# Performance work log

Measured on AMD Instinct MI355X. Metric: run time of the kernel, lower is better.

The kernel has to match this reference:

```python
import jax, jax.numpy as jnp
import numpy as np
from jax.scipy.special import logsumexp

VOCAB, NLABEL, NSTATE = 32000, 16, 64
BATCH, MAXLEN = 512, 512


def setup_inputs() -> dict:
    key = jax.random.key(0)
    k1, k2, k3, k4, k5 = jax.random.split(key, 5)
    sentences = jax.random.randint(k1, (BATCH, MAXLEN), 0, VOCAB)
    length = jax.random.randint(k2, (BATCH,), 1, MAXLEN + 1)  # valid lengths in [1, MAXLEN]
    # parameters, uniform(-0.5, 0.5) as in reset_parameter()
    emb = jax.random.uniform(k3, (VOCAB, NSTATE), minval=-0.5, maxval=0.5, dtype=jnp.float32)
    transition = jax.random.uniform(k4, (NSTATE, NSTATE), minval=-0.5, maxval=0.5, dtype=jnp.float32)
    output = jax.random.uniform(k5, (NLABEL, NSTATE), minval=-0.5, maxval=0.5, dtype=jnp.float32)
    return {"sentences": sentences, "length": length, "emb": emb,
            "transition": transition, "output": output}


def reference(sentences, length, emb, transition, output):
    batch = sentences.shape[0]
    # emission log-probs per timestep: [T, B, S]
    emission = jax.nn.log_softmax(emb[sentences.T], axis=-1)
    trans = jax.nn.log_softmax(transition, axis=-1)  # [S, S]

    def step(f, e):
        # log-space matrix-vector product: logsumexp over previous state
        nf = logsumexp(trans[None, :, :] + f[:, None, :], axis=-1) + e  # [B, S]
        return nf, nf

    f0 = emission[0]
    _, rest = jax.lax.scan(step, f0, emission[1:])
    forwards = jnp.concatenate([f0[None], rest], axis=0)  # [T, B, S]
    hidden = forwards[length - 1, jnp.arange(batch)]  # [B, S]
    out_log = jax.nn.log_softmax(output, axis=-1)  # [L, S]
    score = logsumexp(out_log[None, :, :] + hidden[:, None, :], axis=-1)  # [B, L]
    return score
```

## Files before the change

kernel.cpp:

```cpp
#include <hip/hip_runtime.h>
#include <stdint.h>

#define VOCAB  32000
#define NSTATE 64
#define NLABEL 16
#define BATCH  512
#define MAXLEN 512

#define LOG2E 1.44269504088896340736f
#define LN2_D 0.69314718055994530942

typedef float v2f __attribute__((ext_vector_type(2)));

#if defined(__has_builtin) && __has_builtin(__builtin_amdgcn_exp2f)
#define EXP2(x) __builtin_amdgcn_exp2f(x)
#else
#define EXP2(x) exp2f(x)
#endif
#if defined(__has_builtin) && __has_builtin(__builtin_amdgcn_logf)
#define LOG2(x) __builtin_amdgcn_logf(x)
#else
#define LOG2(x) log2f(x)
#endif

#define SBAR() __builtin_amdgcn_sched_barrier(0)

__device__ __forceinline__ float wave_max64(float x) {
#pragma unroll
  for (int off = 32; off > 0; off >>= 1) x = fmaxf(x, __shfl_xor(x, off, 64));
  return x;
}
__device__ __forceinline__ float wave_sum64(float x) {
#pragma unroll
  for (int off = 32; off > 0; off >>= 1) x += __shfl_xor(x, off, 64);
  return x;
}
__device__ __forceinline__ float bcast0(float x) {
  return __uint_as_float(__builtin_amdgcn_readfirstlane(__float_as_uint(x)));
}

__global__ void prep_emb_k(const float* __restrict__ emb, float* __restrict__ emb2) {
  const int w = blockIdx.x * 4 + (threadIdx.x >> 6);
  const int s = threadIdx.x & 63;
  const float v = emb[w * NSTATE + s] * LOG2E;
  const float m = wave_max64(v);
  const float ss = wave_sum64(EXP2(v - m));
  emb2[w * NSTATE + s] = v - m - LOG2(ss);
}

__global__ void prep_mats_k(const float* __restrict__ trans, const float* __restrict__ outp,
                            float* __restrict__ W, float* __restrict__ out2) {
  const int r = blockIdx.x, s = threadIdx.x;
  if (r < NSTATE) {
    const float v = trans[r * NSTATE + s] * LOG2E;
    const float m = wave_max64(v);
    const float ss = wave_sum64(EXP2(v - m));
    W[r * NSTATE + s] = EXP2(v - m - LOG2(ss));
  } else {
    const int l = r - NSTATE;
    const float v = outp[l * NSTATE + s] * LOG2E;
    const float m = wave_max64(v);
    const float ss = wave_sum64(EXP2(v - m));
    out2[l * NSTATE + s] = v - m - LOG2(ss);
  }
}

template <bool PRE>
__global__ __launch_bounds__(64) void iohmm_fwd(
    const int* __restrict__ sents, const int* __restrict__ length,
    const float* __restrict__ emb, const float* __restrict__ trans,
    const float* __restrict__ outp, const float* __restrict__ emb2,
    const float* __restrict__ W, const float* __restrict__ out2,
    float* __restrict__ score) {
  const int b = blockIdx.x;
  const int s = threadIdx.x;
  __shared__ __align__(16) float p_lds[2][NSTATE];
  __shared__ __align__(16) int s_ids[MAXLEN];

  {
    const int4* s4 = reinterpret_cast<const int4*>(sents + b * MAXLEN);
    int4 c0 = s4[s];
    int4 c1 = s4[64 + s];
    reinterpret_cast<int4*>(s_ids)[s] = c0;
    reinterpret_cast<int4*>(s_ids)[64 + s] = c1;
  }

  v2f w2[NSTATE / 2];
  if (PRE) {
#pragma unroll
    for (int j = 0; j < 16; ++j) {
      const float4 q = *reinterpret_cast<const float4*>(W + s * NSTATE + 4 * j);
      w2[2 * j + 0] = v2f{q.x, q.y};
      w2[2 * j + 1] = v2f{q.z, q.w};
    }
  } else {
    float wr[NSTATE];
#pragma unroll
    for (int j = 0; j < 16; ++j) {
      const float4 q = *reinterpret_cast<const float4*>(trans + s * NSTATE + 4 * j);
      wr[4 * j + 0] = q.x * LOG2E; wr[4 * j + 1] = q.y * LOG2E;
      wr[4 * j + 2] = q.z * LOG2E; wr[4 * j + 3] = q.w * LOG2E;
    }
    float m = -1e30f;
#pragma unroll
    for (int j = 0; j < NSTATE; ++j) m = fmaxf(m, wr[j]);
    float ss = 0.f;
#pragma unroll
    for (int j = 0; j < NSTATE; ++j) ss += EXP2(wr[j] - m);
    const float d = m + LOG2(ss);
#pragma unroll
    for (int j = 0; j < NSTATE / 2; ++j)
      w2[j] = v2f{EXP2(wr[2 * j] - d), EXP2(wr[2 * j + 1] - d)};
  }

  const int len = length[b];
  __syncthreads();

  auto EMIT = [&](int t) -> float {
    const int tc = t < MAXLEN ? t : MAXLEN - 1;
    const int id = s_ids[tc];
    return PRE ? emb2[id * NSTATE + s] : emb[id * NSTATE + s] * LOG2E;
  };

  float e0 = EMIT(0);
  if (!PRE) {
    const float dm = wave_max64(e0);
    const float dsum = wave_sum64(EXP2(e0 - dm));
    e0 = e0 - dm - LOG2(dsum);
  }
  const float se0 = bcast0(e0);
  float p = EXP2(e0 - se0);
  double MU = (double)se0;
  int MUi = 0;

  float eA = EMIT(1);
  float eB = EMIT(2);
  float eC = EMIT(3);

  for (int t = 1; t < len; ++t) {
    float* pb = p_lds[t & 1];
    pb[s] = p;
    SBAR();

    const float eN = EMIT(t + 3);

    const float4* pb4 = reinterpret_cast<const float4*>(pb);
    v2f A0{0.f, 0.f}, A1 = A0, A2 = A0, A3 = A0, A4 = A0, A5 = A0, A6 = A0, A7 = A0;
#pragma unroll
    for (int j = 0; j < 4; ++j) {
      const float4 qa = pb4[4 * j + 0];
      const float4 qb = pb4[4 * j + 1];
      const float4 qc = pb4[4 * j + 2];
      const float4 qd = pb4[4 * j + 3];
      A0 = __builtin_elementwise_fma(w2[8 * j + 0], v2f{qa.x, qa.y}, A0);
      A1 = __builtin_elementwise_fma(w2[8 * j + 1], v2f{qa.z, qa.w}, A1);
      A2 = __builtin_elementwise_fma(w2[8 * j + 2], v2f{qb.x, qb.y}, A2);
      A3 = __builtin_elementwise_fma(w2[8 * j + 3], v2f{qb.z, qb.w}, A3);
      A4 = __builtin_elementwise_fma(w2[8 * j + 4], v2f{qc.x, qc.y}, A4);
      A5 = __builtin_elementwise_fma(w2[8 * j + 5], v2f{qc.z, qc.w}, A5);
      A6 = __builtin_elementwise_fma(w2[8 * j + 6], v2f{qd.x, qd.y}, A6);
      A7 = __builtin_elementwise_fma(w2[8 * j + 7], v2f{qd.z, qd.w}, A7);
    }
    const v2f S0 = A0 + A4, S1 = A1 + A5, S2 = A2 + A6, S3 = A3 + A7;
    const v2f T0 = S0 + S2, T1 = S1 + S3;
    const v2f U = T0 + T1;
    const float sum = U.x + U.y;
    SBAR();

    float e;
    if (PRE) {
      e = eA;
    } else {
      const float dm = wave_max64(eA);
      const float dsum = wave_sum64(EXP2(eA - dm));
      e = eA - dm - LOG2(dsum);
    }
    const float se = bcast0(e);
    const float q = EXP2(e - se);
    p = sum * q;

    if ((t & 15) == 0) {
      const uint32_t u = __builtin_amdgcn_readfirstlane(__float_as_uint(p));
      const int ex = (int)((u >> 23) & 255u) - 127;
      const float r = __uint_as_float((uint32_t)(127 - ex) << 23);
      p *= r;
      MUi += ex;
    }

    MU += (double)se;
    eA = eB; eB = eC; eC = eN;
  }

  const float f = LOG2(p);
  const double MUt = MU + (double)MUi;
  for (int l = 0; l < NLABEL; ++l) {
    float y;
    if (PRE) {
      y = out2[l * NSTATE + s] + f;
    } else {
      const float v = outp[l * NSTATE + s] * LOG2E;
      const float lm = wave_max64(v);
      const float lsum = wave_sum64(EXP2(v - lm));
      y = v - lm - LOG2(lsum) + f;
    }
    const float m = wave_max64(y);
    const float ssum = wave_sum64(EXP2(y - m));
    if (s == 0) {
      const double sc = MUt + (double)m + (double)LOG2(ssum);
      score[b * NLABEL + l] = (float)(sc * LN2_D);
    }
  }
}

extern "C" void kernel_launch(void* const* d_in, const int* in_sizes, int n_in,
                              void* d_out, int out_size, void* d_ws, size_t ws_size,
                              hipStream_t stream) {
  const int* sents = (const int*)d_in[0];
  const int* length = (const int*)d_in[1];
  const float* emb = (const float*)d_in[2];
  const float* trans = (const float*)d_in[3];
  const float* outp = (const float*)d_in[4];
  float* score = (float*)d_out;

  const size_t emb2_bytes = (size_t)VOCAB * NSTATE * sizeof(float);
  const size_t W_off = emb2_bytes;
  const size_t out2_off = W_off + NSTATE * NSTATE * sizeof(float);
  const size_t need = out2_off + NLABEL * NSTATE * sizeof(float);

  if (ws_size >= need) {
    float* emb2 = (float*)d_ws;
    float* W = (float*)((char*)d_ws + W_off);
    float* out2 = (float*)((char*)d_ws + out2_off);
    prep_emb_k<<<VOCAB / 4, 256, 0, stream>>>(emb, emb2);
    prep_mats_k<<<NSTATE + NLABEL, 64, 0, stream>>>(trans, outp, W, out2);
    iohmm_fwd<true><<<BATCH, 64, 0, stream>>>(sents, length, emb, trans, outp,
                                              emb2, W, out2, score);
  } else {
    iohmm_fwd<false><<<BATCH, 64, 0, stream>>>(sents, length, emb, trans, outp,
                                               nullptr, nullptr, nullptr, score);
  }
}
```

Measured before the change: 269.8 us.

## Precompute per-step emission factors and process two sequences per wave

Adds a prepass that gathers the emission log-probs for every (batch, timestep), converts them to linear-scale factors laid out transposed in chunks of 16 steps, and separately sums the per-step max offsets in double. The main recurrence then streams these contiguous float4 chunks with double-buffered prefetch and runs two batch elements per 64-thread block, interleaving two independent dot products to hide LDS and dependency latency. This removes the per-step dependent gather of emb2 from the serial loop. In exchange it needs a large extra workspace (about 64 MB of qT) plus two extra kernel launches, and the grid drops to 256 blocks, which run to the longer of each pair's lengths.

```diff
diff --git a/kernel.cpp b/kernel.cpp
--- a/kernel.cpp
+++ b/kernel.cpp
@@ -6,6 +6,7 @@
 #define NLABEL 16
 #define BATCH  512
 #define MAXLEN 512
+#define NCHUNK (MAXLEN / 16)
 
 #define LOG2E 1.44269504088896340736f
 #define LN2_D 0.69314718055994530942
@@ -37,6 +38,13 @@
 }
 __device__ __forceinline__ float bcast0(float x) {
   return __uint_as_float(__builtin_amdgcn_readfirstlane(__float_as_uint(x)));
+}
+__device__ __forceinline__ double shfl_xor_d(double x, int off) {
+  union { double d; int i[2]; } u;
+  u.d = x;
+  u.i[0] = __shfl_xor(u.i[0], off, 64);
+  u.i[1] = __shfl_xor(u.i[1], off, 64);
+  return u.d;
 }
 
 __global__ void prep_emb_k(const float* __restrict__ emb, float* __restrict__ emb2) {
@@ -65,8 +73,218 @@
   }
 }
 
+__global__ void prep_gather_k(const int* __restrict__ sents,
+                              const float* __restrict__ emb2,
+                              float* __restrict__ qT, float* __restrict__ mu) {
+  const int b = blockIdx.x >> 3;
+  const int tile = blockIdx.x & 7;
+  const int s = threadIdx.x;
+  __shared__ float tileb[64][65];
+
+  const int* sentrow = sents + b * MAXLEN + tile * 64;
+#pragma unroll 4
+  for (int tt = 0; tt < 64; ++tt) {
+    const int id = sentrow[tt];
+    const float e = emb2[id * NSTATE + s];
+    const float e0 = bcast0(e);
+    tileb[tt][s] = EXP2(e - e0);
+    if (s == 0) mu[b * MAXLEN + tile * 64 + tt] = e;
+  }
+  __syncthreads();
+
+  const int lt = s;
+  const int chunk = tile * 4 + (lt >> 4);
+  const int tc = lt & 15;
+  float* dst = qT + ((size_t)(b * NCHUNK + chunk) * NSTATE) * 16 + tc;
+#pragma unroll 8
+  for (int i = 0; i < NSTATE; ++i) {
+    dst[(size_t)i * 16] = tileb[lt][i];
+  }
+}
+
+__global__ void prep_musum_k(const float* __restrict__ mu, const int* __restrict__ length,
+                             double* __restrict__ musum) {
+  const int b = blockIdx.x;
+  const int lane = threadIdx.x;
+  const int len = length[b];
+  double acc = 0.0;
+#pragma unroll
+  for (int k = 0; k < 8; ++k) {
+    const int t = k * 64 + lane;
+    const float v = mu[b * MAXLEN + t];
+    if (t < len) acc += (double)v;
+  }
+#pragma unroll
+  for (int off = 32; off > 0; off >>= 1) acc += shfl_xor_d(acc, off);
+  if (lane == 0) musum[b] = acc;
+}
+
+__device__ __forceinline__ float dot64(const float* __restrict__ pl,
+                                       const v2f* __restrict__ w2) {
+  const float4* pb4 = reinterpret_cast<const float4*>(pl);
+  v2f A0{0.f, 0.f}, A1 = A0, A2 = A0, A3 = A0, A4 = A0, A5 = A0, A6 = A0, A7 = A0;
+#pragma unroll
+  for (int j = 0; j < 4; ++j) {
+    const float4 qa = pb4[4 * j + 0];
+    const float4 qb = pb4[4 * j + 1];
+    const float4 qc = pb4[4 * j + 2];
+    const float4 qd = pb4[4 * j + 3];
+    A0 = __builtin_elementwise_fma(w2[8 * j + 0], v2f{qa.x, qa.y}, A0);
+    A1 = __builtin_elementwise_fma(w2[8 * j + 1], v2f{qa.z, qa.w}, A1);
+    A2 = __builtin_elementwise_fma(w2[8 * j + 2], v2f{qb.x, qb.y}, A2);
+    A3 = __builtin_elementwise_fma(w2[8 * j + 3], v2f{qb.z, qb.w}, A3);
+    A4 = __builtin_elementwise_fma(w2[8 * j + 4], v2f{qc.x, qc.y}, A4);
+    A5 = __builtin_elementwise_fma(w2[8 * j + 5], v2f{qc.z, qc.w}, A5);
+    A6 = __builtin_elementwise_fma(w2[8 * j + 6], v2f{qd.x, qd.y}, A6);
+    A7 = __builtin_elementwise_fma(w2[8 * j + 7], v2f{qd.z, qd.w}, A7);
+  }
+  const v2f S0 = A0 + A4, S1 = A1 + A5, S2 = A2 + A6, S3 = A3 + A7;
+  const v2f T0 = S0 + S2, T1 = S1 + S3;
+  const v2f U = T0 + T1;
+  return U.x + U.y;
+}
+
+__global__ __launch_bounds__(64, 1) void iohmm_fwd3(
+    const int* __restrict__ length, const float* __restrict__ W,
+    const float* __restrict__ out2, const float* __restrict__ qT,
+    const double* __restrict__ musum, float* __restrict__ score) {
+  const int b0 = blockIdx.x * 2;
+  const int b1 = b0 + 1;
+  const int s = threadIdx.x;
+  __shared__ __align__(16) float pl0[NSTATE];
+  __shared__ __align__(16) float pl1[NSTATE];
+
+  v2f w2[NSTATE / 2];
+#pragma unroll
+  for (int j = 0; j < 16; ++j) {
+    const float4 q = *reinterpret_cast<const float4*>(W + s * NSTATE + 4 * j);
+    w2[2 * j + 0] = v2f{q.x, q.y};
+    w2[2 * j + 1] = v2f{q.z, q.w};
+  }
+
+  const int len0 = length[b0];
+  const int len1 = length[b1];
+  const int lmax = len0 > len1 ? len0 : len1;
+  const int nch = (lmax + 15) >> 4;
+
+  const float4* q0b = reinterpret_cast<const float4*>(qT) +
+                      ((size_t)b0 * NCHUNK * NSTATE + s) * 4;
+  const float4* q1b = reinterpret_cast<const float4*>(qT) +
+                      ((size_t)b1 * NCHUNK * NSTATE + s) * 4;
+
+  float pA, pB;
+  int mu0i = 0, mu1i = 0;
+
+  auto dostep = [&](int t, float q0v, float q1v, bool rn) {
+    pl0[s] = pA;
+    pl1[s] = pB;
+    SBAR();
+    const float s0 = dot64(pl0, w2);
+    const float s1 = dot64(pl1, w2);
+    SBAR();
+    if (t < len0) {
+      pA = s0 * q0v;
+      if (rn) {
+        const uint32_t u = __builtin_amdgcn_readfirstlane(__float_as_uint(pA));
+        const int ex = (int)((u >> 23) & 255u) - 127;
+        pA *= __uint_as_float((uint32_t)(127 - ex) << 23);
+        mu0i += ex;
+      }
+    }
+    if (t < len1) {
+      pB = s1 * q1v;
+      if (rn) {
+        const uint32_t u = __builtin_amdgcn_readfirstlane(__float_as_uint(pB));
+        const int ex = (int)((u >> 23) & 255u) - 127;
+        pB *= __uint_as_float((uint32_t)(127 - ex) << 23);
+        mu1i += ex;
+      }
+    }
+  };
+
+  auto do16 = [&](int c, const float4& P0, const float4& P1, const float4& P2,
+                  const float4& P3, const float4& R0, const float4& R1,
+                  const float4& R2, const float4& R3, bool skip0) {
+    const int t0 = c * 16;
+    if (!skip0) dostep(t0 + 0, P0.x, R0.x, true);
+    dostep(t0 + 1, P0.y, R0.y, false);
+    dostep(t0 + 2, P0.z, R0.z, false);
+    dostep(t0 + 3, P0.w, R0.w, false);
+    dostep(t0 + 4, P1.x, R1.x, true);
+    dostep(t0 + 5, P1.y, R1.y, false);
+    dostep(t0 + 6, P1.z, R1.z, false);
+    dostep(t0 + 7, P1.w, R1.w, false);
+    dostep(t0 + 8, P2.x, R2.x, true);
+    dostep(t0 + 9, P2.y, R2.y, false);
+    dostep(t0 + 10, P2.z, R2.z, false);
+    dostep(t0 + 11, P2.w, R2.w, false);
+    dostep(t0 + 12, P3.x, R3.x, true);
+    dostep(t0 + 13, P3.y, R3.y, false);
+    dostep(t0 + 14, P3.z, R3.z, false);
+    dostep(t0 + 15, P3.w, R3.w, false);
+  };
+
+  float4 A00, A01, A02, A03, B00, B01, B02, B03;
+  float4 A10, A11, A12, A13, B10, B11, B12, B13;
+#define LOADC0(c, r0, r1, r2, r3) { const float4* p4_ = q0b + (size_t)(c) * (NSTATE * 4); \
+    r0 = p4_[0]; r1 = p4_[1]; r2 = p4_[2]; r3 = p4_[3]; }
+#define LOADC1(c, r0, r1, r2, r3) { const float4* p4_ = q1b + (size_t)(c) * (NSTATE * 4); \
+    r0 = p4_[0]; r1 = p4_[1]; r2 = p4_[2]; r3 = p4_[3]; }
+
+  LOADC0(0, A00, A01, A02, A03);
+  LOADC1(0, A10, A11, A12, A13);
+  {
+    const int c1 = 1 < NCHUNK ? 1 : NCHUNK - 1;
+    LOADC0(c1, B00, B01, B02, B03);
+    LOADC1(c1, B10, B11, B12, B13);
+  }
+
+  pA = A00.x;
+  pB = A10.x;
+
+  for (int c = 0; c < nch; c += 2) {
+    do16(c, A00, A01, A02, A03, A10, A11, A12, A13, c == 0);
+    {
+      int cn = c + 2; if (cn >= NCHUNK) cn = NCHUNK - 1;
+      LOADC0(cn, A00, A01, A02, A03);
+      LOADC1(cn, A10, A11, A12, A13);
+    }
+    if (c + 1 < nch) do16(c + 1, B00, B01, B02, B03, B10, B11, B12, B13, false);
+    {
+      int cn = c + 3; if (cn >= NCHUNK) cn = NCHUNK - 1;
+      LOADC0(cn, B00, B01, B02, B03);
+      LOADC1(cn, B10, B11, B12, B13);
+    }
+  }
+#undef LOADC0
+#undef LOADC1
+
+  {
+    const float f = LOG2(pA);
+    const double base = musum[b0] + (double)mu0i;
+    for (int l = 0; l < NLABEL; ++l) {
+      const float y = out2[l * NSTATE + s] + f;
+      const float m = wave_max64(y);
+      const float ssum = wave_sum64(EXP2(y - m));
+      if (s == 0)
+        score[b0 * NLABEL + l] = (float)((base + (double)m + (double)LOG2(ssum)) * LN2_D);
+    }
+  }
+  {
+    const float f = LOG2(pB);
+    const double base = musum[b1] + (double)mu1i;
+    for (int l = 0; l < NLABEL; ++l) {
+      const float y = out2[l * NSTATE + s] + f;
+      const float m = wave_max64(y);
+      const float ssum = wave_sum64(EXP2(y - m));
+      if (s == 0)
+        score[b1 * NLABEL + l] = (float)((base + (double)m + (double)LOG2(ssum)) * LN2_D);
+    }
+  }
+}
+
 template <bool PRE>
-__global__ __launch_bounds__(64) void iohmm_fwd(
+__global__ __launch_bounds__(64, 1) void iohmm_fwd(
     const int* __restrict__ sents, const int* __restrict__ length,
     const float* __restrict__ emb, const float* __restrict__ trans,
     const float* __restrict__ outp, const float* __restrict__ emb2,
@@ -76,7 +294,6 @@
   const int s = threadIdx.x;
   __shared__ __align__(16) float p_lds[2][NSTATE];
   __shared__ __align__(16) int s_ids[MAXLEN];
-
   {
     const int4* s4 = reinterpret_cast<const int4*>(sents + b * MAXLEN);
     int4 c0 = s4[s];
@@ -84,7 +301,6 @@
     reinterpret_cast<int4*>(s_ids)[s] = c0;
     reinterpret_cast<int4*>(s_ids)[64 + s] = c1;
   }
-
   v2f w2[NSTATE / 2];
   if (PRE) {
 #pragma unroll
@@ -112,16 +328,13 @@
     for (int j = 0; j < NSTATE / 2; ++j)
       w2[j] = v2f{EXP2(wr[2 * j] - d), EXP2(wr[2 * j + 1] - d)};
   }
-
   const int len = length[b];
   __syncthreads();
-
   auto EMIT = [&](int t) -> float {
     const int tc = t < MAXLEN ? t : MAXLEN - 1;
     const int id = s_ids[tc];
     return PRE ? emb2[id * NSTATE + s] : emb[id * NSTATE + s] * LOG2E;
   };
-
   float e0 = EMIT(0);
   if (!PRE) {
     const float dm = wave_max64(e0);
@@ -132,41 +345,14 @@
   float p = EXP2(e0 - se0);
   double MU = (double)se0;
   int MUi = 0;
-
-  float eA = EMIT(1);
-  float eB = EMIT(2);
-  float eC = EMIT(3);
-
+  float eA = EMIT(1), eB = EMIT(2), eC = EMIT(3);
   for (int t = 1; t < len; ++t) {
     float* pb = p_lds[t & 1];
     pb[s] = p;
     SBAR();
-
     const float eN = EMIT(t + 3);
-
-    const float4* pb4 = reinterpret_cast<const float4*>(pb);
-    v2f A0{0.f, 0.f}, A1 = A0, A2 = A0, A3 = A0, A4 = A0, A5 = A0, A6 = A0, A7 = A0;
-#pragma unroll
-    for (int j = 0; j < 4; ++j) {
-      const float4 qa = pb4[4 * j + 0];
-      const float4 qb = pb4[4 * j + 1];
-      const float4 qc = pb4[4 * j + 2];
-      const float4 qd = pb4[4 * j + 3];
-      A0 = __builtin_elementwise_fma(w2[8 * j + 0], v2f{qa.x, qa.y}, A0);
-      A1 = __builtin_elementwise_fma(w2[8 * j + 1], v2f{qa.z, qa.w}, A1);
-      A2 = __builtin_elementwise_fma(w2[8 * j + 2], v2f{qb.x, qb.y}, A2);
-      A3 = __builtin_elementwise_fma(w2[8 * j + 3], v2f{qb.z, qb.w}, A3);
-      A4 = __builtin_elementwise_fma(w2[8 * j + 4], v2f{qc.x, qc.y}, A4);
-      A5 = __builtin_elementwise_fma(w2[8 * j + 5], v2f{qc.z, qc.w}, A5);
-      A6 = __builtin_elementwise_fma(w2[8 * j + 6], v2f{qd.x, qd.y}, A6);
-      A7 = __builtin_elementwise_fma(w2[8 * j + 7], v2f{qd.z, qd.w}, A7);
-    }
-    const v2f S0 = A0 + A4, S1 = A1 + A5, S2 = A2 + A6, S3 = A3 + A7;
-    const v2f T0 = S0 + S2, T1 = S1 + S3;
-    const v2f U = T0 + T1;
-    const float sum = U.x + U.y;
+    const float sum = dot64(pb, w2);
     SBAR();
-
     float e;
     if (PRE) {
       e = eA;
@@ -178,19 +364,15 @@
     const float se = bcast0(e);
     const float q = EXP2(e - se);
     p = sum * q;
-
     if ((t & 15) == 0) {
       const uint32_t u = __builtin_amdgcn_readfirstlane(__float_as_uint(p));
       const int ex = (int)((u >> 23) & 255u) - 127;
-      const float r = __uint_as_float((uint32_t)(127 - ex) << 23);
-      p *= r;
+      p *= __uint_as_float((uint32_t)(127 - ex) << 23);
       MUi += ex;
     }
-
     MU += (double)se;
     eA = eB; eB = eC; eC = eN;
   }
-
   const float f = LOG2(p);
   const double MUt = MU + (double)MUi;
   for (int l = 0; l < NLABEL; ++l) {
@@ -222,15 +404,38 @@
   const float* outp = (const float*)d_in[4];
   float* score = (float*)d_out;
 
-  const size_t emb2_bytes = (size_t)VOCAB * NSTATE * sizeof(float);
-  const size_t W_off = emb2_bytes;
-  const size_t out2_off = W_off + NSTATE * NSTATE * sizeof(float);
-  const size_t need = out2_off + NLABEL * NSTATE * sizeof(float);
-
-  if (ws_size >= need) {
-    float* emb2 = (float*)d_ws;
+  const size_t emb2_off = 0;
+  const size_t emb2_sz = (size_t)VOCAB * NSTATE * sizeof(float);
+  const size_t qT_off = emb2_off + emb2_sz;
+  const size_t qT_sz = (size_t)BATCH * NCHUNK * NSTATE * 16 * sizeof(float);
+  const size_t mu_off = qT_off + qT_sz;
+  const size_t mu_sz = (size_t)BATCH * MAXLEN * sizeof(float);
+  const size_t musum_off = mu_off + mu_sz;
+  const size_t musum_sz = (size_t)BATCH * sizeof(double);
+  const size_t W_off = musum_off + musum_sz;
+  const size_t W_sz = NSTATE * NSTATE * sizeof(float);
+  const size_t out2_off = W_off + W_sz;
+  const size_t out2_sz = NLABEL * NSTATE * sizeof(float);
+  const size_t need2 = out2_off + out2_sz;
+
+  const size_t need1 = emb2_sz + W_sz + out2_sz;
+
+  if (ws_size >= need2) {
+    float* emb2 = (float*)((char*)d_ws + emb2_off);
+    float* qT = (float*)((char*)d_ws + qT_off);
+    float* mu = (float*)((char*)d_ws + mu_off);
+    double* musum = (double*)((char*)d_ws + musum_off);
     float* W = (float*)((char*)d_ws + W_off);
     float* out2 = (float*)((char*)d_ws + out2_off);
+    prep_emb_k<<<VOCAB / 4, 256, 0, stream>>>(emb, emb2);
+    prep_mats_k<<<NSTATE + NLABEL, 64, 0, stream>>>(trans, outp, W, out2);
+    prep_gather_k<<<BATCH * 8, 64, 0, stream>>>(sents, emb2, qT, mu);
+    prep_musum_k<<<BATCH, 64, 0, stream>>>(mu, length, musum);
+    iohmm_fwd3<<<BATCH / 2, 64, 0, stream>>>(length, W, out2, qT, musum, score);
+  } else if (ws_size >= need1) {
+    float* emb2 = (float*)d_ws;
+    float* W = (float*)((char*)d_ws + emb2_sz);
+    float* out2 = (float*)((char*)d_ws + emb2_sz + W_sz);
     prep_emb_k<<<VOCAB / 4, 256, 0, stream>>>(emb, emb2);
     prep_mats_k<<<NSTATE + NLABEL, 64, 0, stream>>>(trans, outp, W, out2);
     iohmm_fwd<true><<<BATCH, 64, 0, stream>>>(sents, length, emb, trans, outp,
```

After: 300.6 us. +11.4%, slower.

## Parallelize forward recursion over time chunks with bf16 MFMA transfer-matrix products

Applied to the files above, without the earlier changes.

Splits each sequence into 8 chunks of 64 steps, and each chunk's workgroup builds the 64x64 product of scaled transition matrices with bf16 MFMA in LDS. A second kernel chains the chunk matrices against the state vector, and a separate pass precomputes each sequence's sum of emission normalizers in double. This trades the 512-step serial dependency per sequence for 8x more parallel blocks doing matrix-matrix work, adding workspace traffic for the per-chunk matrices. It also brings bf16 rounding into the recursion, which can cost accuracy. The fallback kernel also drops the emission prefetch pipeline.

```diff
diff --git a/kernel.cpp b/kernel.cpp
--- a/kernel.cpp
+++ b/kernel.cpp
@@ -6,11 +6,15 @@
 #define NLABEL 16
 #define BATCH  512
 #define MAXLEN 512
+#define CHUNK  64
+#define NC     (MAXLEN / CHUNK)
 
 #define LOG2E 1.44269504088896340736f
 #define LN2_D 0.69314718055994530942
 
-typedef float v2f __attribute__((ext_vector_type(2)));
+typedef float  f32x4  __attribute__((ext_vector_type(4)));
+typedef short  bf16x8 __attribute__((ext_vector_type(8)));
+typedef float  v2f    __attribute__((ext_vector_type(2)));
 
 #if defined(__has_builtin) && __has_builtin(__builtin_amdgcn_exp2f)
 #define EXP2(x) __builtin_amdgcn_exp2f(x)
@@ -23,8 +27,6 @@
 #define LOG2(x) log2f(x)
 #endif
 
-#define SBAR() __builtin_amdgcn_sched_barrier(0)
-
 __device__ __forceinline__ float wave_max64(float x) {
 #pragma unroll
   for (int off = 32; off > 0; off >>= 1) x = fmaxf(x, __shfl_xor(x, off, 64));
@@ -38,6 +40,21 @@
 __device__ __forceinline__ float bcast0(float x) {
   return __uint_as_float(__builtin_amdgcn_readfirstlane(__float_as_uint(x)));
 }
+__device__ __forceinline__ double shfl_xor_d(double x, int off) {
+  union { double d; int i[2]; } u;
+  u.d = x;
+  u.i[0] = __shfl_xor(u.i[0], off, 64);
+  u.i[1] = __shfl_xor(u.i[1], off, 64);
+  return u.d;
+}
+__device__ __forceinline__ unsigned short f2bf(float x) {
+  uint32_t u = __float_as_uint(x);
+  return (unsigned short)((u + 0x7FFFu + ((u >> 16) & 1u)) >> 16);
+}
+__device__ __forceinline__ float bf2f(unsigned short h) {
+  return __uint_as_float(((uint32_t)h) << 16);
+}
+__device__ __forceinline__ int swz(int a) { return a ^ (((a >> 7) & 7) << 4); }
 
 __global__ void prep_emb_k(const float* __restrict__ emb, float* __restrict__ emb2) {
   const int w = blockIdx.x * 4 + (threadIdx.x >> 6);
@@ -65,35 +82,202 @@
   }
 }
 
-template <bool PRE>
-__global__ __launch_bounds__(64) void iohmm_fwd(
+__global__ void prep_wfrag_k(const float* __restrict__ W, bf16x8* __restrict__ Wb) {
+  const int l = threadIdx.x;
+  const int l15 = l & 15, lh = l >> 4;
+#pragma unroll
+  for (int mi = 0; mi < 4; ++mi)
+#pragma unroll
+    for (int ks = 0; ks < 2; ++ks) {
+      bf16x8 v;
+#pragma unroll
+      for (int i = 0; i < 8; ++i)
+        v[i] = (short)f2bf(W[(mi * 16 + l15) * 64 + ks * 32 + 8 * lh + i]);
+      Wb[(mi * 2 + ks) * 64 + l] = v;
+    }
+}
+
+__global__ void prep_musum2_k(const int* __restrict__ sents, const float* __restrict__ emb2,
+                              const int* __restrict__ length, double* __restrict__ musum) {
+  const int b = blockIdx.x;
+  const int l = threadIdx.x;
+  const int len = length[b];
+  double acc = 0.0;
+#pragma unroll
+  for (int k = 0; k < 8; ++k) {
+    const int t = k * 64 + l;
+    const int id = sents[b * MAXLEN + t];
+    const float e0 = emb2[id * NSTATE];
+    if (t < len) acc += (double)e0;
+  }
+#pragma unroll
+  for (int off = 32; off > 0; off >>= 1) acc += shfl_xor_d(acc, off);
+  if (l == 0) musum[b] = acc;
+}
+
+__global__ __launch_bounds__(64, 2) void phaseA_k(
+    const int* __restrict__ sents, const int* __restrict__ length,
+    const float* __restrict__ emb2, const bf16x8* __restrict__ Wb,
+    unsigned short* __restrict__ Mout, int* __restrict__ Mexp) {
+  const int tid = blockIdx.x;
+  const int b = tid >> 3;
+  const int c = tid & 7;
+  const int l = threadIdx.x;
+  const int l15 = l & 15, lh = l >> 4;
+
+  __shared__ __align__(16) unsigned short MT[4096];
+  __shared__ __align__(16) float q_lds[NSTATE];
+  __shared__ __align__(16) int ids[CHUNK];
+
+  ids[l] = sents[b * MAXLEN + c * CHUNK + l];
+
+  bf16x8 wf[4][2];
+#pragma unroll
+  for (int mi = 0; mi < 4; ++mi)
+#pragma unroll
+    for (int ks = 0; ks < 2; ++ks)
+      wf[mi][ks] = Wb[(mi * 2 + ks) * 64 + l];
+
+  {
+    const int4 z{0, 0, 0, 0};
+#pragma unroll
+    for (int k = 0; k < 8; ++k)
+      *reinterpret_cast<int4*>(reinterpret_cast<char*>(MT) + k * 1024 + l * 16) = z;
+    const int dbyte = swz(128 * l + 2 * l);
+    *reinterpret_cast<unsigned short*>(reinterpret_cast<char*>(MT) + dbyte) = 0x3F80u;
+  }
+
+  const int len = length[b];
+  const int t0 = c * CHUNK;
+  const int start = (c == 0) ? 1 : t0;
+  const int end_ = ((len - 1) < (t0 + CHUNK - 1)) ? (len - 1) : (t0 + CHUNK - 1);
+  const int K = end_ - start + 1;
+  int MUc = 0;
+
+  if (K > 0) {
+    int idx = start - t0;
+    int idc = ids[idx];
+    float e_cur = emb2[idc * NSTATE + l];
+    float rnorm = 1.0f;
+    bool rn_pending = false;
+
+    for (int j = 0; j < K; ++j) {
+      const int idxn = (j + 1 < K) ? (idx + 1) : idx;
+      const int idn = ids[idxn];
+      const float e_nxt = emb2[idn * NSTATE + l];
+
+      const float se = bcast0(e_cur);
+      q_lds[l] = EXP2(e_cur - se);
+
+      float samp = 0.f;
+#pragma unroll
+      for (int pass = 0; pass < 2; ++pass) {
+        bf16x8 mf[2][2];
+#pragma unroll
+        for (int ks = 0; ks < 2; ++ks)
+#pragma unroll
+          for (int nn = 0; nn < 2; ++nn) {
+            const int n = (pass * 2 + nn) * 16 + l15;
+            const int byte = swz(128 * n + 64 * ks + 16 * lh);
+            mf[ks][nn] = *reinterpret_cast<const bf16x8*>(
+                reinterpret_cast<const char*>(MT) + byte);
+          }
+#pragma unroll
+        for (int mi = 0; mi < 4; ++mi) {
+          f32x4 qf = *reinterpret_cast<const f32x4*>(q_lds + mi * 16 + 4 * lh);
+          if (rn_pending) qf *= rnorm;
+#pragma unroll
+          for (int nn = 0; nn < 2; ++nn) {
+            f32x4 acc{0.f, 0.f, 0.f, 0.f};
+            acc = __builtin_amdgcn_mfma_f32_16x16x32_bf16(wf[mi][0], mf[0][nn], acc, 0, 0, 0);
+            acc = __builtin_amdgcn_mfma_f32_16x16x32_bf16(wf[mi][1], mf[1][nn], acc, 0, 0, 0);
+            acc *= qf;
+            if (pass == 0 && nn == 0 && mi == 0) samp = acc.x;
+            const uint32_t lo = (uint32_t)f2bf(acc.x) | ((uint32_t)f2bf(acc.y) << 16);
+            const uint32_t hi = (uint32_t)f2bf(acc.z) | ((uint32_t)f2bf(acc.w) << 16);
+            const int n = (pass * 2 + nn) * 16 + l15;
+            const int wbyte = swz(128 * n + 2 * (mi * 16 + 4 * lh));
+            *reinterpret_cast<uint2*>(reinterpret_cast<char*>(MT) + wbyte) = uint2{lo, hi};
+          }
+        }
+      }
+      rn_pending = false;
+      if (((j & 7) == 7) && (j + 1 < K)) {
+        const uint32_t u = __builtin_amdgcn_readfirstlane(__float_as_uint(samp));
+        const int ex = (int)((u >> 23) & 255u) - 127;
+        rnorm = __uint_as_float((uint32_t)(127 - ex) << 23);
+        rn_pending = true;
+        MUc += ex;
+      }
+      e_cur = e_nxt;
+      idx = idxn;
+    }
+  }
+
+  unsigned short* dst = Mout + (size_t)tid * 4096;
+#pragma unroll
+  for (int k = 0; k < 8; ++k) {
+    const int4 v = *reinterpret_cast<const int4*>(
+        reinterpret_cast<const char*>(MT) + k * 1024 + l * 16);
+    *reinterpret_cast<int4*>(reinterpret_cast<char*>(dst) + k * 1024 + l * 16) = v;
+  }
+  if (l == 0) Mexp[tid] = MUc;
+}
+
+__global__ __launch_bounds__(64) void phaseB_k(
+    const int* __restrict__ sents, const int* __restrict__ length,
+    const float* __restrict__ emb2, const float* __restrict__ out2,
+    const unsigned short* __restrict__ Mout, const int* __restrict__ Mexp,
+    const double* __restrict__ musum, float* __restrict__ score) {
+  const int b = blockIdx.x;
+  const int l = threadIdx.x;
+  const int len = length[b];
+
+  const int id0 = sents[b * MAXLEN];
+  const float e0 = emb2[id0 * NSTATE + l];
+  const float se0 = bcast0(e0);
+  float p = EXP2(e0 - se0);
+  int MUi = 0;
+
+  for (int c = 0; c < NC && c * CHUNK < len; ++c) {
+    const unsigned short* M = Mout + ((size_t)(b * NC + c)) * 4096;
+    float acc = 0.f;
+#pragma unroll 8
+    for (int n = 0; n < 64; ++n) {
+      const float pn = __shfl(p, n, 64);
+      const int byte = swz(128 * n + 2 * l);
+      const unsigned short h = *reinterpret_cast<const unsigned short*>(
+          reinterpret_cast<const char*>(M) + byte);
+      acc = fmaf(bf2f(h), pn, acc);
+    }
+    p = acc;
+    MUi += Mexp[b * NC + c];
+    const uint32_t u = __builtin_amdgcn_readfirstlane(__float_as_uint(p));
+    const int ex = (int)((u >> 23) & 255u) - 127;
+    p *= __uint_as_float((uint32_t)(127 - ex) << 23);
+    MUi += ex;
+  }
+
+  const float f = LOG2(p);
+  const double base = musum[b] + (double)MUi;
+  for (int ll = 0; ll < NLABEL; ++ll) {
+    const float y = out2[ll * NSTATE + l] + f;
+    const float m = wave_max64(y);
+    const float ssum = wave_sum64(EXP2(y - m));
+    if (l == 0)
+      score[b * NLABEL + ll] = (float)((base + (double)m + (double)LOG2(ssum)) * LN2_D);
+  }
+}
+
+__global__ __launch_bounds__(64, 1) void iohmm_fwd_fb(
     const int* __restrict__ sents, const int* __restrict__ length,
     const float* __restrict__ emb, const float* __restrict__ trans,
-    const float* __restrict__ outp, const float* __restrict__ emb2,
-    const float* __restrict__ W, const float* __restrict__ out2,
-    float* __restrict__ score) {
+    const float* __restrict__ outp, float* __restrict__ score) {
   const int b = blockIdx.x;
   const int s = threadIdx.x;
   __shared__ __align__(16) float p_lds[2][NSTATE];
-  __shared__ __align__(16) int s_ids[MAXLEN];
-
+  v2f w2[NSTATE / 2];
   {
-    const int4* s4 = reinterpret_cast<const int4*>(sents + b * MAXLEN);
-    int4 c0 = s4[s];
-    int4 c1 = s4[64 + s];
-    reinterpret_cast<int4*>(s_ids)[s] = c0;
-    reinterpret_cast<int4*>(s_ids)[64 + s] = c1;
-  }
-
-  v2f w2[NSTATE / 2];
-  if (PRE) {
-#pragma unroll
-    for (int j = 0; j < 16; ++j) {
-      const float4 q = *reinterpret_cast<const float4*>(W + s * NSTATE + 4 * j);
-      w2[2 * j + 0] = v2f{q.x, q.y};
-      w2[2 * j + 1] = v2f{q.z, q.w};
-    }
-  } else {
     float wr[NSTATE];
 #pragma unroll
     for (int j = 0; j < 16; ++j) {
@@ -112,18 +296,13 @@
     for (int j = 0; j < NSTATE / 2; ++j)
       w2[j] = v2f{EXP2(wr[2 * j] - d), EXP2(wr[2 * j + 1] - d)};
   }
-
   const int len = length[b];
-  __syncthreads();
-
   auto EMIT = [&](int t) -> float {
     const int tc = t < MAXLEN ? t : MAXLEN - 1;
-    const int id = s_ids[tc];
-    return PRE ? emb2[id * NSTATE + s] : emb[id * NSTATE + s] * LOG2E;
+    return emb[sents[b * MAXLEN + tc] * NSTATE + s] * LOG2E;
   };
-
   float e0 = EMIT(0);
-  if (!PRE) {
+  {
     const float dm = wave_max64(e0);
     const float dsum = wave_sum64(EXP2(e0 - dm));
     e0 = e0 - dm - LOG2(dsum);
@@ -132,83 +311,49 @@
   float p = EXP2(e0 - se0);
   double MU = (double)se0;
   int MUi = 0;
-
-  float eA = EMIT(1);
-  float eB = EMIT(2);
-  float eC = EMIT(3);
-
   for (int t = 1; t < len; ++t) {
     float* pb = p_lds[t & 1];
     pb[s] = p;
-    SBAR();
-
-    const float eN = EMIT(t + 3);
-
+    __builtin_amdgcn_sched_barrier(0);
+    const float eR = EMIT(t);
     const float4* pb4 = reinterpret_cast<const float4*>(pb);
-    v2f A0{0.f, 0.f}, A1 = A0, A2 = A0, A3 = A0, A4 = A0, A5 = A0, A6 = A0, A7 = A0;
-#pragma unroll
-    for (int j = 0; j < 4; ++j) {
-      const float4 qa = pb4[4 * j + 0];
-      const float4 qb = pb4[4 * j + 1];
-      const float4 qc = pb4[4 * j + 2];
-      const float4 qd = pb4[4 * j + 3];
-      A0 = __builtin_elementwise_fma(w2[8 * j + 0], v2f{qa.x, qa.y}, A0);
-      A1 = __builtin_elementwise_fma(w2[8 * j + 1], v2f{qa.z, qa.w}, A1);
-      A2 = __builtin_elementwise_fma(w2[8 * j + 2], v2f{qb.x, qb.y}, A2);
-      A3 = __builtin_elementwise_fma(w2[8 * j + 3], v2f{qb.z, qb.w}, A3);
-      A4 = __builtin_elementwise_fma(w2[8 * j + 4], v2f{qc.x, qc.y}, A4);
-      A5 = __builtin_elementwise_fma(w2[8 * j + 5], v2f{qc.z, qc.w}, A5);
-      A6 = __builtin_elementwise_fma(w2[8 * j + 6], v2f{qd.x, qd.y}, A6);
-      A7 = __builtin_elementwise_fma(w2[8 * j + 7], v2f{qd.z, qd.w}, A7);
-    }
-    const v2f S0 = A0 + A4, S1 = A1 + A5, S2 = A2 + A6, S3 = A3 + A7;
-    const v2f T0 = S0 + S2, T1 = S1 + S3;
-    const v2f U = T0 + T1;
+    v2f A0{0.f, 0.f}, A1 = A0, A2 = A0, A3 = A0;
+#pragma unroll
+    for (int j = 0; j < 8; ++j) {
+      const float4 qa = pb4[2 * j + 0];
+      const float4 qb = pb4[2 * j + 1];
+      A0 = __builtin_elementwise_fma(w2[4 * j + 0], v2f{qa.x, qa.y}, A0);
+      A1 = __builtin_elementwise_fma(w2[4 * j + 1], v2f{qa.z, qa.w}, A1);
+      A2 = __builtin_elementwise_fma(w2[4 * j + 2], v2f{qb.x, qb.y}, A2);
+      A3 = __builtin_elementwise_fma(w2[4 * j + 3], v2f{qb.z, qb.w}, A3);
+    }
+    const v2f S0 = A0 + A2, S1 = A1 + A3;
+    const v2f U = S0 + S1;
     const float sum = U.x + U.y;
-    SBAR();
-
-    float e;
-    if (PRE) {
-      e = eA;
-    } else {
-      const float dm = wave_max64(eA);
-      const float dsum = wave_sum64(EXP2(eA - dm));
-      e = eA - dm - LOG2(dsum);
-    }
+    const float dm = wave_max64(eR);
+    const float dsum = wave_sum64(EXP2(eR - dm));
+    const float e = eR - dm - LOG2(dsum);
     const float se = bcast0(e);
-    const float q = EXP2(e - se);
-    p = sum * q;
-
+    p = sum * EXP2(e - se);
     if ((t & 15) == 0) {
       const uint32_t u = __builtin_amdgcn_readfirstlane(__float_as_uint(p));
       const int ex = (int)((u >> 23) & 255u) - 127;
-      const float r = __uint_as_float((uint32_t)(127 - ex) << 23);
-      p *= r;
+      p *= __uint_as_float((uint32_t)(127 - ex) << 23);
       MUi += ex;
     }
-
     MU += (double)se;
-    eA = eB; eB = eC; eC = eN;
-  }
-
+  }
   const float f = LOG2(p);
   const double MUt = MU + (double)MUi;
-  for (int l = 0; l < NLABEL; ++l) {
-    float y;
-    if (PRE) {
-      y = out2[l * NSTATE + s] + f;
-    } else {
-      const float v = outp[l * NSTATE + s] * LOG2E;
-      const float lm = wave_max64(v);
-      const float lsum = wave_sum64(EXP2(v - lm));
-      y = v - lm - LOG2(lsum) + f;
-    }
+  for (int ll = 0; ll < NLABEL; ++ll) {
+    const float v = outp[ll * NSTATE + s] * LOG2E;
+    const float lm = wave_max64(v);
+    const float lsum = wave_sum64(EXP2(v - lm));
+    const float y = v - lm - LOG2(lsum) + f;
     const float m = wave_max64(y);
     const float ssum = wave_sum64(EXP2(y - m));
-    if (s == 0) {
-      const double sc = MUt + (double)m + (double)LOG2(ssum);
-      score[b * NLABEL + l] = (float)(sc * LN2_D);
-    }
+    if (s == 0)
+      score[b * NLABEL + ll] = (float)((MUt + (double)m + (double)LOG2(ssum)) * LN2_D);
   }
 }
 
@@ -222,21 +367,38 @@
   const float* outp = (const float*)d_in[4];
   float* score = (float*)d_out;
 
-  const size_t emb2_bytes = (size_t)VOCAB * NSTATE * sizeof(float);
-  const size_t W_off = emb2_bytes;
-  const size_t out2_off = W_off + NSTATE * NSTATE * sizeof(float);
-  const size_t need = out2_off + NLABEL * NSTATE * sizeof(float);
+  const size_t emb2_off = 0;
+  const size_t emb2_sz = (size_t)VOCAB * NSTATE * sizeof(float);
+  const size_t W_off = emb2_off + emb2_sz;
+  const size_t W_sz = NSTATE * NSTATE * sizeof(float);
+  const size_t out2_off = W_off + W_sz;
+  const size_t out2_sz = NLABEL * NSTATE * sizeof(float);
+  const size_t Wb_off = out2_off + out2_sz;
+  const size_t Wb_sz = 8 * 64 * 16;
+  const size_t musum_off = Wb_off + Wb_sz;
+  const size_t musum_sz = BATCH * sizeof(double);
+  const size_t Mexp_off = musum_off + musum_sz;
+  const size_t Mexp_sz = (size_t)BATCH * NC * sizeof(int);
+  const size_t Mout_off = Mexp_off + Mexp_sz;
+  const size_t Mout_sz = (size_t)BATCH * NC * 4096 * sizeof(unsigned short);
+  const size_t need = Mout_off + Mout_sz;
 
   if (ws_size >= need) {
-    float* emb2 = (float*)d_ws;
+    float* emb2 = (float*)((char*)d_ws + emb2_off);
     float* W = (float*)((char*)d_ws + W_off);
     float* out2 = (float*)((char*)d_ws + out2_off);
+    bf16x8* Wb = (bf16x8*)((char*)d_ws + Wb_off);
+    double* musum = (double*)((char*)d_ws + musum_off);
+    int* Mexp = (int*)((char*)d_ws + Mexp_off);
+    unsigned short* Mout = (unsigned short*)((char*)d_ws + Mout_off);
+
     prep_emb_k<<<VOCAB / 4, 256, 0, stream>>>(emb, emb2);
     prep_mats_k<<<NSTATE + NLABEL, 64, 0, stream>>>(trans, outp, W, out2);
-    iohmm_fwd<true><<<BATCH, 64, 0, stream>>>(sents, length, emb, trans, outp,
-                                              emb2, W, out2, score);
+    prep_wfrag_k<<<1, 64, 0, stream>>>(W, Wb);
+    prep_musum2_k<<<BATCH, 64, 0, stream>>>(sents, emb2, length, musum);
+    phaseA_k<<<BATCH * NC, 64, 0, stream>>>(sents, length, emb2, Wb, Mout, Mexp);
+    phaseB_k<<<BATCH, 64, 0, stream>>>(sents, length, emb2, out2, Mout, Mexp, musum, score);
   } else {
-    iohmm_fwd<false><<<BATCH, 64, 0, stream>>>(sents, length, emb, trans, outp,
-                                               nullptr, nullptr, nullptr, score);
-  }
-}
+    iohmm_fwd_fb<<<BATCH, 64, 0, stream>>>(sents, length, emb, trans, outp, score);
+  }
+}
```

After: 304.4 us. 12.8% more time.
